# Kernel optimization log

Hardware: AMD Instinct MI355X
Metric: run time of the kernel (lower is better)

Reference implementation:

```python
import jax, jax.numpy as jnp
import numpy as np

N = 100000      # nodes
E = 1600000     # edges (avg degree 16)
DIN = 3         # input_dim (xyz coords)
DOUT = 64       # output_dim
EPS = 1e-5      # LayerNorm eps


def setup_inputs() -> dict:
    key = jax.random.key(0)
    ks = jax.random.split(key, 6)
    x = jax.random.normal(ks[0], (N, DIN), jnp.float32)
    edge_index = jax.random.randint(ks[1], (2, E), 0, N, dtype=jnp.int64)
    # li1: Linear(DIN, DOUT)
    W1 = jax.random.normal(ks[2], (DIN, DOUT), jnp.float32) / np.sqrt(DIN)
    b1 = jnp.zeros((DOUT,), jnp.float32)
    # gcn1: GCNConv(DOUT, DOUT) -> weight + bias
    Wg = jax.random.normal(ks[3], (DOUT, DOUT), jnp.float32) / np.sqrt(DOUT)
    bg = jnp.zeros((DOUT,), jnp.float32)
    # norm1d: LayerNorm(2*DOUT)
    gamma = jnp.ones((2 * DOUT,), jnp.float32)
    beta = jnp.zeros((2 * DOUT,), jnp.float32)
    return {"x": x, "edge_index": edge_index, "W1": W1, "b1": b1,
            "Wg": Wg, "bg": bg, "gamma": gamma, "beta": beta}


def reference(x, edge_index, W1, b1, Wg, bg, gamma, beta):
    n = x.shape[0]
    # li1 + act
    h = jax.nn.relu(x @ W1 + b1)                       # [N, DOUT]
    # GCNConv: add self loops, symmetric normalization D^-1/2 (A+I) D^-1/2
    loops = jnp.arange(n, dtype=edge_index.dtype)
    src = jnp.concatenate([edge_index[0], loops])      # [E+N]
    dst = jnp.concatenate([edge_index[1], loops])      # [E+N]
    deg = jax.ops.segment_sum(jnp.ones_like(dst, h.dtype), dst, num_segments=n)
    dinv = jnp.where(deg > 0, jax.lax.rsqrt(jnp.maximum(deg, 1.0)), 0.0)
    norm = dinv[src] * dinv[dst]                       # [E+N]
    hg = h @ Wg                                        # [N, DOUT]
    agg = jax.ops.segment_sum(hg[src] * norm[:, None], dst, num_segments=n)
    h2 = jax.nn.relu(agg + bg)                         # [N, DOUT]
    # concat + LayerNorm(2*DOUT)
    cat = jnp.concatenate([h, h2], axis=1)             # [N, 2*DOUT]
    mu = jnp.mean(cat, axis=-1, keepdims=True)
    var = jnp.mean(jnp.square(cat - mu), axis=-1, keepdims=True)
    return (cat - mu) * jax.lax.rsqrt(var + EPS) * gamma + beta
```

## Files before the change

kernel.cpp:

```cpp
#include <hip/hip_runtime.h>
#include <math.h>

#define N_NODES 100000
#define N_EDGES 1600000
#define EPS_    1e-5f
#define PAD     64
#define SCOL    48

#define NB_BUILD 6250
#define LIN_CHUNKS 1563


__device__ __forceinline__ float bf2f(unsigned short u) {
    union { unsigned int i; float f; } v; v.i = (unsigned int)u << 16; return v.f;
}
__device__ __forceinline__ unsigned short f2bf(float f) {
    union { float f; unsigned int i; } v; v.f = f;
    unsigned int b = v.i + 0x7FFFu + ((v.i >> 16) & 1u);
    return (unsigned short)(b >> 16);
}

__global__ void build_lin_kernel(const int* __restrict__ src,
                                 const int* __restrict__ dst,
                                 const float* __restrict__ x,
                                 const float* __restrict__ W1,
                                 const float* __restrict__ b1,
                                 const float* __restrict__ Wg,
                                 int* __restrict__ cnt,
                                 int* __restrict__ ell,
                                 unsigned short* __restrict__ hb_g)
{
    const int tl   = threadIdx.x;
    const int gtid = blockIdx.x * 256 + tl;

    const int d   = dst[gtid];
    const int s   = src[gtid];
    const int pos = atomicAdd(&cnt[d], 1);

    const int chunk = blockIdx.x * 4 + (tl >> 6);
    if (chunk < LIN_CHUNKS) {
        const int lane = tl & 63;
        const int n    = chunk * 64 + lane;
        const bool act = (n < N_NODES);
        float x0 = 0.f, x1 = 0.f, x2 = 0.f;
        if (act) { x0 = x[n * 3]; x1 = x[n * 3 + 1]; x2 = x[n * 3 + 2]; }

        float acc[64];
#pragma unroll
        for (int c = 0; c < 64; ++c) acc[c] = 0.f;

#pragma unroll 2
        for (int k = 0; k < 64; ++k) {
            const float w0 = W1[k];
            const float w1 = W1[64 + k];
            const float w2 = W1[128 + k];
            const float bb = b1[k];
            float hk = fmaf(x0, w0, fmaf(x1, w1, fmaf(x2, w2, bb)));
            hk = fmaxf(hk, 0.f);
            const float* __restrict__ wr = Wg + k * 64;
#pragma unroll
            for (int c = 0; c < 64; ++c) acc[c] = fmaf(hk, wr[c], acc[c]);
        }

        if (act) {
            unsigned int o[32];
#pragma unroll
            for (int c = 0; c < 32; ++c)
                o[c] = (unsigned int)f2bf(acc[2 * c])
                     | ((unsigned int)f2bf(acc[2 * c + 1]) << 16);
            uint4* __restrict__ dp = (uint4*)(hb_g + (size_t)n * 64);
#pragma unroll
            for (int q = 0; q < 8; ++q)
                dp[q] = make_uint4(o[4 * q], o[4 * q + 1], o[4 * q + 2], o[4 * q + 3]);
        }
    }

    if (pos < PAD) ell[d * PAD + pos] = s;
}

__global__ void scale_kernel(const int* __restrict__ cnt,
                             unsigned int* __restrict__ g2)
{
    const int t = blockIdx.x * blockDim.x + threadIdx.x;
    if (t >= N_NODES * 32) return;
    const int node = t >> 5;
    const float di = rsqrtf((float)(cnt[node] + 1));
    const unsigned int v = g2[t];
    const float lo = bf2f((unsigned short)(v & 0xFFFFu)) * di;
    const float hi = bf2f((unsigned short)(v >> 16)) * di;
    g2[t] = (unsigned int)f2bf(lo) | ((unsigned int)f2bf(hi) << 16);
}

__global__ void gather_final_kernel(const unsigned short* __restrict__ hb_g,
                                    const int* __restrict__ cnt,
                                    const int* __restrict__ ell,
                                    const float* __restrict__ x,
                                    const float* __restrict__ W1,
                                    const float* __restrict__ b1,
                                    const float* __restrict__ bg,
                                    const float* __restrict__ gamma,
                                    const float* __restrict__ beta,
                                    float* __restrict__ out)
{
    __shared__ int sell[64 * SCOL];
    __shared__ int lcnt[64];
    const int tl = threadIdx.x;
    const int b  = blockIdx.x;
    const int nb = b * 64;

    if (tl < 64) {
        const int n = nb + tl;
        lcnt[tl] = (n < N_NODES) ? cnt[n] : 0;
    }
    {
        const int r = tl >> 2;
        const int q = tl & 3;
        const int nr = nb + r;
        if (nr < N_NODES) {
            const int4* __restrict__ grow = (const int4*)(ell + (size_t)nr * PAD);
            int4* __restrict__ srow = (int4*)(sell + r * SCOL);
            srow[q]     = grow[q];
            srow[q + 4] = grow[q + 4];
            srow[q + 8] = grow[q + 8];
        }
    }
    __syncthreads();

    const int lane = tl & 63;
    const int w    = tl >> 6;
    const float w0 = W1[lane], w1 = W1[64 + lane], w2 = W1[128 + lane];
    const float bb1 = b1[lane];
    const float bgl = bg[lane];
    const float g0 = gamma[lane], g1 = gamma[64 + lane];
    const float be0 = beta[lane], be1 = beta[64 + lane];

    for (int nl = w; nl < 64; nl += 4) {
        const int n = nb + nl;
        if (n >= N_NODES) break;

        const int c    = lcnt[nl];
        const float di = rsqrtf((float)(c + 1));
        const int deg  = (c < PAD) ? c : PAD;
        const int dstg = (deg < SCOL) ? deg : SCOL;
        const int* row = sell + nl * SCOL;

        const float xx0 = x[n * 3], xx1 = x[n * 3 + 1], xx2 = x[n * 3 + 2];
        float acc = bf2f(hb_g[(size_t)n * 64 + lane]);

        int j = 0;
        for (; j + 8 <= dstg; j += 8) {
            const int s0 = row[j + 0], s1 = row[j + 1], s2 = row[j + 2], s3 = row[j + 3];
            const int s4 = row[j + 4], s5 = row[j + 5], s6 = row[j + 6], s7 = row[j + 7];
            const float a0 = bf2f(hb_g[(size_t)s0 * 64 + lane]);
            const float a1 = bf2f(hb_g[(size_t)s1 * 64 + lane]);
            const float a2 = bf2f(hb_g[(size_t)s2 * 64 + lane]);
            const float a3 = bf2f(hb_g[(size_t)s3 * 64 + lane]);
            const float a4 = bf2f(hb_g[(size_t)s4 * 64 + lane]);
            const float a5 = bf2f(hb_g[(size_t)s5 * 64 + lane]);
            const float a6 = bf2f(hb_g[(size_t)s6 * 64 + lane]);
            const float a7 = bf2f(hb_g[(size_t)s7 * 64 + lane]);
            acc += ((a0 + a1) + (a2 + a3)) + ((a4 + a5) + (a6 + a7));
        }
        if (j + 4 <= dstg) {
            const int s0 = row[j + 0], s1 = row[j + 1], s2 = row[j + 2], s3 = row[j + 3];
            acc += (bf2f(hb_g[(size_t)s0 * 64 + lane]) + bf2f(hb_g[(size_t)s1 * 64 + lane]))
                 + (bf2f(hb_g[(size_t)s2 * 64 + lane]) + bf2f(hb_g[(size_t)s3 * 64 + lane]));
            j += 4;
        }
        for (; j < dstg; ++j) acc += bf2f(hb_g[(size_t)row[j] * 64 + lane]);
        for (; j < deg; ++j)
            acc += bf2f(hb_g[(size_t)ell[(size_t)n * PAD + j] * 64 + lane]);

        float h  = fmaxf(fmaf(xx0, w0, fmaf(xx1, w1, fmaf(xx2, w2, bb1))), 0.f);
        float h2 = fmaxf(fmaf(di, acc, bgl), 0.f);

        float sum = h + h2;
#pragma unroll
        for (int o = 32; o > 0; o >>= 1) sum += __shfl_xor(sum, o, 64);
        const float mu = sum * (1.0f / 128.0f);

        const float dA = h  - mu;
        const float dB = h2 - mu;
        float vs = dA * dA + dB * dB;
#pragma unroll
        for (int o = 32; o > 0; o >>= 1) vs += __shfl_xor(vs, o, 64);
        const float rr = rsqrtf(vs * (1.0f / 128.0f) + EPS_);

        out[(size_t)n * 128 + lane]      = dA * rr * g0 + be0;
        out[(size_t)n * 128 + 64 + lane] = dB * rr * g1 + be1;
    }
}

extern "C" void kernel_launch(void* const* d_in, const int* in_sizes, int n_in,
                              void* d_out, int out_size, void* d_ws, size_t ws_size,
                              hipStream_t stream)
{
    const float* x     = (const float*)d_in[0];
    const int*   edge  = (const int*)  d_in[1];
    const float* W1    = (const float*)d_in[2];
    const float* b1    = (const float*)d_in[3];
    const float* Wg    = (const float*)d_in[4];
    const float* bg    = (const float*)d_in[5];
    const float* gamma = (const float*)d_in[6];
    const float* beta  = (const float*)d_in[7];
    float*       out   = (float*)d_out;

    char*  ws  = (char*)d_ws;
    size_t p   = 0;
    unsigned short* hb_g = (unsigned short*)(ws + p); p += (size_t)N_NODES * 64 * sizeof(unsigned short);
    int*            ell  = (int*)           (ws + p); p += (size_t)N_NODES * PAD * sizeof(int);
    int*            cnt  = (int*)           (ws + p);

    const int* src = edge;
    const int* dst = edge + N_EDGES;

    hipMemsetAsync(cnt, 0, (size_t)N_NODES * sizeof(int), stream);

    build_lin_kernel<<<NB_BUILD, 256, 0, stream>>>(src, dst, x, W1, b1, Wg,
                                                   cnt, ell, hb_g);
    scale_kernel<<<(N_NODES * 32 + 255) / 256, 256, 0, stream>>>(cnt, (unsigned int*)hb_g);
    gather_final_kernel<<<(N_NODES + 63) / 64, 256, 0, stream>>>(hb_g, cnt, ell,
                                                                 x, W1, b1,
                                                                 bg, gamma, beta, out);
}
```

Measured before the change: 266.0 us.

## Split edge scatter from linear kernel and compute two nodes per thread

```diff
diff --git a/kernel.cpp b/kernel.cpp
--- a/kernel.cpp
+++ b/kernel.cpp
@@ -7,8 +7,9 @@
 #define PAD     64
 #define SCOL    48
 
-#define NB_BUILD 6250
-#define LIN_CHUNKS 1563
+#define NB_EDGE  6250
+#define NB_LIN   391
+#define LIN_CHUNKS 782
 
 
 __device__ __forceinline__ float bf2f(unsigned short u) {
@@ -20,62 +21,89 @@
     return (unsigned short)(b >> 16);
 }
 
-__global__ void build_lin_kernel(const int* __restrict__ src,
-                                 const int* __restrict__ dst,
-                                 const float* __restrict__ x,
-                                 const float* __restrict__ W1,
-                                 const float* __restrict__ b1,
-                                 const float* __restrict__ Wg,
-                                 int* __restrict__ cnt,
-                                 int* __restrict__ ell,
-                                 unsigned short* __restrict__ hb_g)
-{
-    const int tl   = threadIdx.x;
-    const int gtid = blockIdx.x * 256 + tl;
-
-    const int d   = dst[gtid];
-    const int s   = src[gtid];
-    const int pos = atomicAdd(&cnt[d], 1);
-
-    const int chunk = blockIdx.x * 4 + (tl >> 6);
-    if (chunk < LIN_CHUNKS) {
-        const int lane = tl & 63;
-        const int n    = chunk * 64 + lane;
-        const bool act = (n < N_NODES);
-        float x0 = 0.f, x1 = 0.f, x2 = 0.f;
-        if (act) { x0 = x[n * 3]; x1 = x[n * 3 + 1]; x2 = x[n * 3 + 2]; }
-
-        float acc[64];
-#pragma unroll
-        for (int c = 0; c < 64; ++c) acc[c] = 0.f;
-
-#pragma unroll 2
-        for (int k = 0; k < 64; ++k) {
-            const float w0 = W1[k];
-            const float w1 = W1[64 + k];
-            const float w2 = W1[128 + k];
-            const float bb = b1[k];
-            float hk = fmaf(x0, w0, fmaf(x1, w1, fmaf(x2, w2, bb)));
-            hk = fmaxf(hk, 0.f);
-            const float* __restrict__ wr = Wg + k * 64;
-#pragma unroll
-            for (int c = 0; c < 64; ++c) acc[c] = fmaf(hk, wr[c], acc[c]);
-        }
-
-        if (act) {
-            unsigned int o[32];
-#pragma unroll
-            for (int c = 0; c < 32; ++c)
-                o[c] = (unsigned int)f2bf(acc[2 * c])
-                     | ((unsigned int)f2bf(acc[2 * c + 1]) << 16);
-            uint4* __restrict__ dp = (uint4*)(hb_g + (size_t)n * 64);
-#pragma unroll
-            for (int q = 0; q < 8; ++q)
-                dp[q] = make_uint4(o[4 * q], o[4 * q + 1], o[4 * q + 2], o[4 * q + 3]);
-        }
-    }
-
+__global__ void edge_kernel(const int* __restrict__ src,
+                            const int* __restrict__ dst,
+                            int* __restrict__ cnt,
+                            int* __restrict__ ell)
+{
+    const int gtid = blockIdx.x * 256 + threadIdx.x;
+    const int d    = dst[gtid];
+    const int s    = src[gtid];
+    const int pos  = atomicAdd(&cnt[d], 1);
     if (pos < PAD) ell[d * PAD + pos] = s;
+}
+
+__global__ void lin_kernel(const float* __restrict__ x,
+                           const float* __restrict__ W1,
+                           const float* __restrict__ b1,
+                           const float* __restrict__ Wg,
+                           unsigned short* __restrict__ hb_g)
+{
+    const int tl    = threadIdx.x;
+    const int chunk = blockIdx.x * 2 + (tl >> 6);
+    if (chunk >= LIN_CHUNKS) return;
+
+    const int lane = tl & 63;
+    const int nA   = chunk * 128 + lane;
+    const int nB   = nA + 64;
+    const bool actA = (nA < N_NODES);
+    const bool actB = (nB < N_NODES);
+
+    float xA0 = 0.f, xA1 = 0.f, xA2 = 0.f, xB0 = 0.f, xB1 = 0.f, xB2 = 0.f;
+    if (actA) { xA0 = x[nA * 3]; xA1 = x[nA * 3 + 1]; xA2 = x[nA * 3 + 2]; }
+    if (actB) { xB0 = x[nB * 3]; xB1 = x[nB * 3 + 1]; xB2 = x[nB * 3 + 2]; }
+
+    float accA[64], accB[64];
+#pragma unroll
+    for (int c = 0; c < 64; ++c) { accA[c] = 0.f; accB[c] = 0.f; }
+
+    for (int k = 0; k < 64; ++k) {
+        const float w0 = W1[k];
+        const float w1 = W1[64 + k];
+        const float w2 = W1[128 + k];
+        const float bb = b1[k];
+        float hA = fmaf(xA0, w0, fmaf(xA1, w1, fmaf(xA2, w2, bb)));
+        float hB = fmaf(xB0, w0, fmaf(xB1, w1, fmaf(xB2, w2, bb)));
+        hA = fmaxf(hA, 0.f);
+        hB = fmaxf(hB, 0.f);
+
+        const float4* __restrict__ row4 = (const float4*)(Wg + k * 64);
+#pragma unroll
+        for (int c4 = 0; c4 < 16; ++c4) {
+            const float4 wv = row4[c4];
+            accA[4 * c4 + 0] = fmaf(hA, wv.x, accA[4 * c4 + 0]);
+            accA[4 * c4 + 1] = fmaf(hA, wv.y, accA[4 * c4 + 1]);
+            accA[4 * c4 + 2] = fmaf(hA, wv.z, accA[4 * c4 + 2]);
+            accA[4 * c4 + 3] = fmaf(hA, wv.w, accA[4 * c4 + 3]);
+            accB[4 * c4 + 0] = fmaf(hB, wv.x, accB[4 * c4 + 0]);
+            accB[4 * c4 + 1] = fmaf(hB, wv.y, accB[4 * c4 + 1]);
+            accB[4 * c4 + 2] = fmaf(hB, wv.z, accB[4 * c4 + 2]);
+            accB[4 * c4 + 3] = fmaf(hB, wv.w, accB[4 * c4 + 3]);
+        }
+    }
+
+    if (actA) {
+        unsigned int o[32];
+#pragma unroll
+        for (int c = 0; c < 32; ++c)
+            o[c] = (unsigned int)f2bf(accA[2 * c])
+                 | ((unsigned int)f2bf(accA[2 * c + 1]) << 16);
+        uint4* __restrict__ dp = (uint4*)(hb_g + (size_t)nA * 64);
+#pragma unroll
+        for (int q = 0; q < 8; ++q)
+            dp[q] = make_uint4(o[4 * q], o[4 * q + 1], o[4 * q + 2], o[4 * q + 3]);
+    }
+    if (actB) {
+        unsigned int o[32];
+#pragma unroll
+        for (int c = 0; c < 32; ++c)
+            o[c] = (unsigned int)f2bf(accB[2 * c])
+                 | ((unsigned int)f2bf(accB[2 * c + 1]) << 16);
+        uint4* __restrict__ dp = (uint4*)(hb_g + (size_t)nB * 64);
+#pragma unroll
+        for (int q = 0; q < 8; ++q)
+            dp[q] = make_uint4(o[4 * q], o[4 * q + 1], o[4 * q + 2], o[4 * q + 3]);
+    }
 }
 
 __global__ void scale_kernel(const int* __restrict__ cnt,
@@ -216,8 +244,8 @@
 
     hipMemsetAsync(cnt, 0, (size_t)N_NODES * sizeof(int), stream);
 
-    build_lin_kernel<<<NB_BUILD, 256, 0, stream>>>(src, dst, x, W1, b1, Wg,
-                                                   cnt, ell, hb_g);
+    edge_kernel<<<NB_EDGE, 256, 0, stream>>>(src, dst, cnt, ell);
+    lin_kernel <<<NB_LIN,  128, 0, stream>>>(x, W1, b1, Wg, hb_g);
     scale_kernel<<<(N_NODES * 32 + 255) / 256, 256, 0, stream>>>(cnt, (unsigned int*)hb_g);
     gather_final_kernel<<<(N_NODES + 63) / 64, 256, 0, stream>>>(hb_g, cnt, ell,
                                                                  x, W1, b1,
```

Measured after the change: 343.6 us. 1.29x slower.
